# Performance work log

Measured on AMD Instinct MI355X. Metric: run time of the kernel, lower is better.

## Reference

```python
import jax, jax.numpy as jnp
from jax import lax
import numpy as np

N_TIMESTEPS = 100000


def setup_inputs() -> dict:
    key = jax.random.key(0)
    k1, k2 = jax.random.split(key)
    params = jax.random.normal(k1, (11,), dtype=jnp.float32)
    epsilons = jax.random.normal(k2, (N_TIMESTEPS,), dtype=jnp.float32)
    return {"params": params, "epsilons": epsilons}


def reference(params, epsilons):
    # params: [log_beta, g1..g4, b1..b4, log_sigma, log_r]
    beta = jnp.exp(params[0])
    g = params[1:5]          # (4,)
    b = params[5:9]          # (4,)
    sigma = jnp.exp(params[-2])
    r = jnp.exp(params[-1])
    R = 1.0 + r

    # Faithful to the torch code: at step t (with x = hstack(zeros(3), x_0..x_{t-1})),
    # x[t-1], x[t-2], x[t-3] resolve to x_{t-4}, x_{t-5}, x_{t-6} (zeros for t<4/5/6;
    # the t=0 negative-index case also yields zeros, so a zero-initialized lag buffer
    # reproduces it exactly). Carry = (x_{t-6}, x_{t-5}, x_{t-4}, x_{t-3}, x_{t-2}, x_{t-1}).
    def step(carry, eps_t):
        xm6 = carry[0]
        xm5 = carry[1]
        xm4 = carry[2]
        exponent = beta * (xm4 - R * xm5) * (g * xm6 + b - R * xm5)  # (4,)
        w = jax.nn.softmax(exponent, axis=-1)                         # (4,)
        mean = jnp.sum(w * (g * xm4 + b))
        x_t = (mean + eps_t * sigma) / R
        new_carry = jnp.concatenate([carry[1:], x_t[None]])
        return new_carry, x_t

    init = jnp.zeros(6, dtype=params.dtype)
    _, xs = lax.scan(step, init, epsilons)
    return xs  # shape (n_timesteps,), equals x[3:] of the torch module
```

## Files before the change

### kernel.cpp

```cpp
#include <hip/hip_runtime.h>
#include <math.h>


constexpr int NT = 100000;
constexpr int NS = NT / 4;
constexpr int BURN_CHUNK  = 32768;
constexpr int BURN_CHUNKS = 60;

#define QP_XOR1  0xB1
#define QP_XOR2  0x4E
#define QP_XOR3  0x1B
#define ROW_SHR4  0x114
#define ROW_SHR8  0x118
#define ROW_SHL8  0x108
#define ROW_SHL12 0x10C

template <int CTRL>
__device__ __forceinline__ float dppf(float x) {
    return __int_as_float(
        __builtin_amdgcn_update_dpp(0, __float_as_int(x), CTRL, 0xf, 0xf, true));
}

__global__ __launch_bounds__(256) void bh_wave(const float* __restrict__ params,
                                               const float* __restrict__ eps,
                                               float* __restrict__ out,
                                               int* __restrict__ flag) {
    if (blockIdx.x != 0) {
        float a = 1.0f + (float)threadIdx.x;
        float c = 0.9999f;
        float a2 = 2.0f;
        for (int ch = 0; ch < BURN_CHUNKS; ++ch) {
            for (int i = 0; i < BURN_CHUNK; ++i) {
                a  = __builtin_fmaf(a,  c, 1.0e-4f);
                a2 = __builtin_fmaf(a2, c, 2.0e-4f);
            }
            if (__hip_atomic_load(flag, __ATOMIC_RELAXED,
                                  __HIP_MEMORY_SCOPE_AGENT)) break;
        }
        asm volatile("" :: "v"(a), "v"(a2));
        return;
    }

    const int tid = threadIdx.x;

    if (tid >= 64) {
        float acc = 0.f;
        const float4* e4p = reinterpret_cast<const float4*>(eps);
        for (int i = tid - 64; i < NT / 4; i += 192) {
            float4 v = e4p[i];
            acc += v.x + v.y + v.z + v.w;
        }
        asm volatile("" :: "v"(acc));
        return;
    }
    if (tid >= 16) return;

    if (tid == 0) {
        __hip_atomic_store(flag, 0, __ATOMIC_RELAXED, __HIP_MEMORY_SCOPE_AGENT);
    }

    const int q = tid >> 2;
    const int j = tid & 3;

    const float beta   = expf(params[0]);
    const float g      = params[1 + j];
    const float b      = params[5 + j];
    const float sigma  = expf(params[9]);
    const float R      = 1.0f + expf(params[10]);
    const float Rinv   = 1.0f / R;
    const float beta2  = beta * 1.4426950408889634f;
    const float A2     = beta2 * Rinv;
    const float nbeta2 = -beta2;
    const float gR     = g * Rinv;

    float z  = 0.f;
    float zp = 0.f;

    float e0 = eps[4 * 0 + q] * sigma, e1 = eps[4 * 1 + q] * sigma;
    float e2 = eps[4 * 2 + q] * sigma, e3 = eps[4 * 3 + q] * sigma;
    float e4 = eps[4 * 4 + q] * sigma, e5 = eps[4 * 5 + q] * sigma;
    float e6 = eps[4 * 6 + q] * sigma, e7 = eps[4 * 7 + q] * sigma;

#define STEP(EV, SS)                                                          \
    {                                                                         \
        float bA  = A2 * z;                     \
        float vv  = __builtin_fmaf(gR, z, b);                                 \
        float xm5 = dppf<ROW_SHR4>(z) + dppf<ROW_SHL12>(zp);                  \
        float xm6 = dppf<ROW_SHR8>(z) + dppf<ROW_SHL8>(zp);                   \
        float u   = __builtin_fmaf(gR, xm6, b);                               \
        float p   = __builtin_fmaf(nbeta2, xm5, bA);                          \
        float qq  = u - xm5;                                                  \
        float x   = p * qq;                                                   \
        float t   = __builtin_amdgcn_exp2f(x);                                \
        float tv  = t * vv;                                                   \
        float ta  = dppf<QP_XOR1>(t);                                         \
        float tb  = dppf<QP_XOR2>(t);                                         \
        float tc  = dppf<QP_XOR3>(t);                                         \
        float va  = dppf<QP_XOR1>(tv);                                        \
        float vb  = dppf<QP_XOR2>(tv);                                        \
        float vc  = dppf<QP_XOR3>(tv);                                        \
        float ts  = (t + ta) + (tb + tc);                  \
        float tvs = (tv + va) + (vb + vc);                                    \
        float rc   = __builtin_amdgcn_rcpf(ts);                               \
        float ynew = __builtin_fmaf(tvs, rc, (EV));                           \
        out[4 * (SS) + q] = ynew * Rinv;                 \
        zp = z; z = ynew;                                                     \
    }

    for (int s = 0; s < NS - 8; s += 8) {
        const int bse = s + 8;
        float n0 = eps[4 * (bse + 0) + q] * sigma;
        float n1 = eps[4 * (bse + 1) + q] * sigma;
        float n2 = eps[4 * (bse + 2) + q] * sigma;
        float n3 = eps[4 * (bse + 3) + q] * sigma;
        float n4 = eps[4 * (bse + 4) + q] * sigma;
        float n5 = eps[4 * (bse + 5) + q] * sigma;
        float n6 = eps[4 * (bse + 6) + q] * sigma;
        float n7 = eps[4 * (bse + 7) + q] * sigma;

        STEP(e0, s + 0);
        STEP(e1, s + 1);
        STEP(e2, s + 2);
        STEP(e3, s + 3);
        STEP(e4, s + 4);
        STEP(e5, s + 5);
        STEP(e6, s + 6);
        STEP(e7, s + 7);

        e0 = n0; e1 = n1; e2 = n2; e3 = n3;
        e4 = n4; e5 = n5; e6 = n6; e7 = n7;
    }
    {
        const int s = NS - 8;
        STEP(e0, s + 0);
        STEP(e1, s + 1);
        STEP(e2, s + 2);
        STEP(e3, s + 3);
        STEP(e4, s + 4);
        STEP(e5, s + 5);
        STEP(e6, s + 6);
        STEP(e7, s + 7);
    }
#undef STEP

    if (tid == 0) {
        __hip_atomic_store(flag, 1, __ATOMIC_RELAXED, __HIP_MEMORY_SCOPE_AGENT);
    }
}

extern "C" void kernel_launch(void* const* d_in, const int* in_sizes, int n_in,
                              void* d_out, int out_size, void* d_ws, size_t ws_size,
                              hipStream_t stream) {
    const float* params = (const float*)d_in[0];
    const float* eps    = (const float*)d_in[1];
    float*       out    = (float*)d_out;
    int*         flag   = (int*)d_ws;
    bh_wave<<<256, 256, 0, stream>>>(params, eps, out, flag);
}
```

Before: 1.705 ms.

## Compute all four softmax terms per lane, dropping cross-lane softmax reduction

Each of the four active lanes now evaluates all four softmax components itself, so the wavefront's work shrinks from 16 lanes to 4. This removes the six quad-permute DPP reductions on the serial critical path. Lag exchange uses row shifts by 1/2/3 lanes instead of 4/8/12. In exchange each lane runs four exp2 calls and about four times the FMA work per step, which lengthens each step's dependency chain slightly but avoids DPP latency.

```diff
diff --git a/kernel.cpp b/kernel.cpp
--- a/kernel.cpp
+++ b/kernel.cpp
@@ -7,13 +7,10 @@
 constexpr int BURN_CHUNK  = 32768;
 constexpr int BURN_CHUNKS = 60;
 
-#define QP_XOR1  0xB1
-#define QP_XOR2  0x4E
-#define QP_XOR3  0x1B
-#define ROW_SHR4  0x114
-#define ROW_SHR8  0x118
-#define ROW_SHL8  0x108
-#define ROW_SHL12 0x10C
+#define ROW_SHR1 0x111
+#define ROW_SHR2 0x112
+#define ROW_SHL2 0x102
+#define ROW_SHL3 0x103
 
 template <int CTRL>
 __device__ __forceinline__ float dppf(float x) {
@@ -53,25 +50,25 @@
         asm volatile("" :: "v"(acc));
         return;
     }
-    if (tid >= 16) return;
+    if (tid >= 4) return;
 
     if (tid == 0) {
         __hip_atomic_store(flag, 0, __ATOMIC_RELAXED, __HIP_MEMORY_SCOPE_AGENT);
     }
 
-    const int q = tid >> 2;
-    const int j = tid & 3;
+    const int q = tid;
 
     const float beta   = expf(params[0]);
-    const float g      = params[1 + j];
-    const float b      = params[5 + j];
+    const float g0 = params[1], g1 = params[2], g2 = params[3], g3 = params[4];
+    const float b0 = params[5], b1 = params[6], b2 = params[7], b3 = params[8];
     const float sigma  = expf(params[9]);
     const float R      = 1.0f + expf(params[10]);
     const float Rinv   = 1.0f / R;
     const float beta2  = beta * 1.4426950408889634f;
     const float A2     = beta2 * Rinv;
     const float nbeta2 = -beta2;
-    const float gR     = g * Rinv;
+    const float gR0 = g0 * Rinv, gR1 = g1 * Rinv;
+    const float gR2 = g2 * Rinv, gR3 = g3 * Rinv;
 
     float z  = 0.f;
     float zp = 0.f;
@@ -83,27 +80,32 @@
 
 #define STEP(EV, SS)                                                          \
     {                                                                         \
-        float bA  = A2 * z;                     \
-        float vv  = __builtin_fmaf(gR, z, b);                                 \
-        float xm5 = dppf<ROW_SHR4>(z) + dppf<ROW_SHL12>(zp);                  \
-        float xm6 = dppf<ROW_SHR8>(z) + dppf<ROW_SHL8>(zp);                   \
-        float u   = __builtin_fmaf(gR, xm6, b);                               \
+        float bA  = A2 * z;                                                   \
+        float vv0 = __builtin_fmaf(gR0, z, b0);                               \
+        float vv1 = __builtin_fmaf(gR1, z, b1);                               \
+        float vv2 = __builtin_fmaf(gR2, z, b2);                               \
+        float vv3 = __builtin_fmaf(gR3, z, b3);                               \
+        float xm5 = dppf<ROW_SHR1>(z) + dppf<ROW_SHL3>(zp);                   \
+        float xm6 = dppf<ROW_SHR2>(z) + dppf<ROW_SHL2>(zp);                   \
         float p   = __builtin_fmaf(nbeta2, xm5, bA);                          \
-        float qq  = u - xm5;                                                  \
-        float x   = p * qq;                                                   \
-        float t   = __builtin_amdgcn_exp2f(x);                                \
-        float tv  = t * vv;                                                   \
-        float ta  = dppf<QP_XOR1>(t);                                         \
-        float tb  = dppf<QP_XOR2>(t);                                         \
-        float tc  = dppf<QP_XOR3>(t);                                         \
-        float va  = dppf<QP_XOR1>(tv);                                        \
-        float vb  = dppf<QP_XOR2>(tv);                                        \
-        float vc  = dppf<QP_XOR3>(tv);                                        \
-        float ts  = (t + ta) + (tb + tc);                  \
-        float tvs = (tv + va) + (vb + vc);                                    \
+        float u0  = __builtin_fmaf(gR0, xm6, b0);                             \
+        float u1  = __builtin_fmaf(gR1, xm6, b1);                             \
+        float u2  = __builtin_fmaf(gR2, xm6, b2);                             \
+        float u3  = __builtin_fmaf(gR3, xm6, b3);                             \
+        float x0  = p * (u0 - xm5);                                           \
+        float x1  = p * (u1 - xm5);                                           \
+        float x2  = p * (u2 - xm5);                                           \
+        float x3  = p * (u3 - xm5);                                           \
+        float t0  = __builtin_amdgcn_exp2f(x0);                               \
+        float t1  = __builtin_amdgcn_exp2f(x1);                               \
+        float t2  = __builtin_amdgcn_exp2f(x2);                               \
+        float t3  = __builtin_amdgcn_exp2f(x3);                               \
+        float ts  = (t0 + t1) + (t2 + t3);                                    \
+        float tvs = (__builtin_fmaf(t0, vv0, t1 * vv1))                       \
+                  + (__builtin_fmaf(t2, vv2, t3 * vv3));                      \
         float rc   = __builtin_amdgcn_rcpf(ts);                               \
         float ynew = __builtin_fmaf(tvs, rc, (EV));                           \
-        out[4 * (SS) + q] = ynew * Rinv;                 \
+        out[4 * (SS) + q] = ynew * Rinv;                                      \
         zp = z; z = ynew;                                                     \
     }
 
```

Result: slower. 2.004 ms (+17.5%).
